# Performance work log

Hardware: AMD Instinct MI355X
Metric: run time of the kernel (lower is better)

## Reference

```python
import jax, jax.numpy as jnp
import numpy as np

B, T, C, H = 2, 4096, 768, 12
D = C // H  # head_dim = 64


def setup_inputs() -> dict:
    key = jax.random.key(0)
    k1, k2, k3 = jax.random.split(key, 3)
    x = jax.random.normal(k1, (B, T, C), dtype=jnp.float32)
    w_qkv = jax.random.normal(k2, (C, 3 * C), dtype=jnp.float32) * (1.0 / np.sqrt(C))
    w_out = jax.random.normal(k3, (C, C), dtype=jnp.float32) * (1.0 / np.sqrt(C))
    return {"x": x, "w_qkv": w_qkv, "w_out": w_out}


def reference(x, w_qkv, w_out):
    b, t, c = x.shape
    qkv = x @ w_qkv                              # (B,T,3C)
    q, k, v = jnp.split(qkv, 3, axis=-1)
    # (B,T,C) -> (B,H,T,D)
    q = q.reshape(b, t, H, D).transpose(0, 2, 1, 3)
    k = k.reshape(b, t, H, D).transpose(0, 2, 1, 3)
    v = v.reshape(b, t, H, D).transpose(0, 2, 1, 3)
    att = jnp.einsum('bhqd,bhkd->bhqk', q, k) / jnp.sqrt(jnp.float32(D))
    causal = jnp.tril(jnp.ones((t, t), dtype=bool))  # True where allowed
    att = jnp.where(causal, att, -jnp.inf)
    att = jax.nn.softmax(att, axis=-1)
    y = jnp.einsum('bhqk,bhkd->bhqd', att, v)        # (B,H,T,D)
    y = y.transpose(0, 2, 1, 3).reshape(b, t, c)
    return y @ w_out
```

## Files before the change

kernel.cpp:

```cpp
#include <hip/hip_runtime.h>
#include <stdint.h>
#include <stddef.h>

#define NB 2
#define NT 4096
#define NC 768
#define NH 12
#define ND 64

typedef unsigned short u16;
typedef __attribute__((ext_vector_type(4))) float f32x4;
typedef __attribute__((ext_vector_type(16))) float f32x16;
typedef __attribute__((ext_vector_type(8))) unsigned short u16x8;
typedef __attribute__((ext_vector_type(4))) unsigned short u16x4;
typedef __attribute__((ext_vector_type(8))) __bf16 bf16x8;
typedef __attribute__((ext_vector_type(4))) unsigned int u32x4;

typedef __attribute__((address_space(1))) const unsigned int gu32;
typedef __attribute__((address_space(3))) unsigned int lu32;

__device__ __forceinline__ u16 f2bf(float f) {
  uint32_t u = __builtin_bit_cast(uint32_t, f);
  u += 0x7FFFu + ((u >> 16) & 1u);
  return (u16)(u >> 16);
}
__device__ __forceinline__ bf16x8 asbf(u16x8 v) { return __builtin_bit_cast(bf16x8, v); }

__device__ __forceinline__ uint32_t pkbf(float a, float b) {
  uint32_t ua = __builtin_bit_cast(uint32_t, a) + 0x8000u;
  uint32_t ub = __builtin_bit_cast(uint32_t, b) + 0x8000u;
  return __builtin_amdgcn_perm(ub, ua, 0x07060302u);
}
__device__ __forceinline__ uint32_t pktr(float a, float b) {
  return __builtin_amdgcn_perm(__builtin_bit_cast(uint32_t, b),
                               __builtin_bit_cast(uint32_t, a), 0x07060302u);
}

#define GLDS(gsrc, ldst) __builtin_amdgcn_global_load_lds( \
    (gu32*)(gsrc), (lu32*)(ldst), 16, 0, 0)

__global__ void k_cast(const float* __restrict__ in, u16* __restrict__ out, int n4) {
  int i = blockIdx.x * blockDim.x + threadIdx.x;
  if (i < n4) {
    f32x4 v = ((const f32x4*)in)[i];
    u16x4 o;
    o[0] = f2bf(v[0]); o[1] = f2bf(v[1]); o[2] = f2bf(v[2]); o[3] = f2bf(v[3]);
    ((u16x4*)out)[i] = o;
  }
}

__global__ void k_transpose(const float* __restrict__ in, u16* __restrict__ out,
                            int R, int Cn) {
  __shared__ float tile[32][33];
  int c0 = blockIdx.x * 32, r0 = blockIdx.y * 32;
  int tx = threadIdx.x & 31, ty = threadIdx.x >> 5;
  for (int i = ty; i < 32; i += 8)
    tile[i][tx] = in[(size_t)(r0 + i) * Cn + c0 + tx];
  __syncthreads();
  for (int i = ty; i < 32; i += 8)
    out[(size_t)(c0 + i) * R + r0 + tx] = f2bf(tile[tx][i]);
}

template <int EPI>
__global__ __launch_bounds__(256, 3)
void k_gemm_bt(const u16* __restrict__ A, const u16* __restrict__ Bt,
               int M, int N, int K,
               u16* __restrict__ o0, u16* __restrict__ o1, u16* __restrict__ o2,
               float* __restrict__ of) {
  __shared__ u16 As[128 * 32];
  __shared__ u16 Bs[128 * 32];
  const int tid = threadIdx.x;
  const int wave = tid >> 6, lane = tid & 63, quad = lane >> 4, lc = lane & 15;
  const int wm = (wave & 1) * 64, wn = (wave >> 1) * 64;
  const int bm = blockIdx.y * 128, bn = blockIdx.x * 128;

  const int sr = tid >> 2;
  const int sc8 = (tid & 3) * 8;
  const u16* ga0 = A + (size_t)(bm + sr) * K + sc8;
  const u16* ga1 = A + (size_t)(bm + 64 + sr) * K + sc8;
  const u16* gb0 = Bt + (size_t)(bn + sr) * K + sc8;
  const u16* gb1 = Bt + (size_t)(bn + 64 + sr) * K + sc8;
  u16* la0 = &As[wave * 512];
  u16* la1 = &As[2048 + wave * 512];
  u16* lb0 = &Bs[wave * 512];
  u16* lb1 = &Bs[2048 + wave * 512];

  f32x4 zv = {0.f, 0.f, 0.f, 0.f};
  f32x4 acc[4][4];
#pragma unroll
  for (int i = 0; i < 4; ++i)
#pragma unroll
    for (int j = 0; j < 4; ++j) acc[i][j] = zv;

  for (int k0 = 0; k0 < K; k0 += 32) {
    __syncthreads();
    GLDS(ga0 + k0, la0);
    GLDS(ga1 + k0, la1);
    GLDS(gb0 + k0, lb0);
    GLDS(gb1 + k0, lb1);
    asm volatile("s_waitcnt vmcnt(0)" ::: "memory");
    __syncthreads();

    bf16x8 af[4], bfv[4];
#pragma unroll
    for (int mi = 0; mi < 4; ++mi)
      af[mi] = asbf(*(const u16x8*)&As[(wm + mi * 16 + lc) * 32 + quad * 8]);
#pragma unroll
    for (int ni = 0; ni < 4; ++ni)
      bfv[ni] = asbf(*(const u16x8*)&Bs[(wn + ni * 16 + lc) * 32 + quad * 8]);
#pragma unroll
    for (int mi = 0; mi < 4; ++mi)
#pragma unroll
      for (int ni = 0; ni < 4; ++ni)
        acc[mi][ni] = __builtin_amdgcn_mfma_f32_16x16x32_bf16(af[mi], bfv[ni],
                                                              acc[mi][ni], 0, 0, 0);
  }

  const int mrow0 = bm + wm + quad * 4;
#pragma unroll
  for (int mi = 0; mi < 4; ++mi) {
    const int mbase = mrow0 + mi * 16;
#pragma unroll
    for (int ni = 0; ni < 4; ++ni) {
      const int n = bn + wn + ni * 16 + lc;
      if (EPI == 0) {
#pragma unroll
        for (int r = 0; r < 4; ++r)
          of[(size_t)(mbase + r) * N + n] = acc[mi][ni][r];
      } else {
        const int sect = n / NC;
        const int wn2 = n - sect * NC;
        const int h = wn2 >> 6, d = wn2 & 63;
        const int b = mbase >> 12;
        const int t = mbase & (NT - 1);
        const float sc = (sect == 0) ? 0.18033688011112042f : 1.0f;
        if (sect == 2) {
          u16x4 pk;
#pragma unroll
          for (int r = 0; r < 4; ++r) pk[r] = f2bf(acc[mi][ni][r]);
          *(u16x4*)&o2[((size_t)(b * NH + h) * ND + d) * NT + t] = pk;
        } else {
          u16* dst = (sect == 0) ? o0 : o1;
#pragma unroll
          for (int r = 0; r < 4; ++r)
            dst[((size_t)(b * NH + h) * NT + (t + r)) * ND + d] =
                f2bf(acc[mi][ni][r] * sc);
        }
      }
    }
  }
}

__device__ __forceinline__ void softpack16(const f32x16& s, int qrel, bool msk,
                                           int l5, float& sl, bf16x8* pf) {
  float e[16];
#pragma unroll
  for (int r = 0; r < 16; ++r) {
    float v = s[r];
    if (msk) {
      int tl = (r & 3) + 8 * (r >> 2) + 4 * l5;
      v = (tl > qrel) ? -1e30f : v;
    }
    e[r] = exp2f(v);
    sl += __builtin_bit_cast(float,
          __builtin_bit_cast(uint32_t, e[r]) & 0xFFFF0000u);
  }
  uint32_t wv[8];
#pragma unroll
  for (int i = 0; i < 8; ++i) wv[i] = pktr(e[2 * i], e[2 * i + 1]);
#pragma unroll
  for (int g = 0; g < 2; ++g) {
    auto r0 = __builtin_amdgcn_permlane32_swap(wv[g * 4 + 0], wv[g * 4 + 2], false, false);
    auto r1 = __builtin_amdgcn_permlane32_swap(wv[g * 4 + 1], wv[g * 4 + 3], false, false);
    u32x4 f = {r0[0], r1[0], r0[1], r1[1]};
    pf[g] = __builtin_bit_cast(bf16x8, f);
  }
}

__global__ __launch_bounds__(256, 3)
void k_attn(const u16* __restrict__ Q, const u16* __restrict__ K,
            const u16* __restrict__ Vt, u16* __restrict__ Y) {
  __shared__ u16 SM[2][64 * 64];
  __shared__ float PL[2][64];
  const int tid = threadIdx.x;
  const int lane = tid & 63, wave = tid >> 6;
  const int l5 = lane >> 5, l31 = lane & 31;
  const int qh = wave & 1, th = wave >> 1;
  const int bh = blockIdx.x % (NB * NH);
  const int qi = 63 - blockIdx.x / (NB * NH);
  const int b = bh / NH, h = bh - b * NH;
  const u16* __restrict__ Qb = Q + (size_t)bh * NT * ND;
  const u16* __restrict__ Kb = K + (size_t)bh * NT * ND;
  const u16* __restrict__ Vb = Vt + (size_t)bh * (size_t)ND * NT;

  const int qg = qi * 64 + qh * 32 + l31;

  bf16x8 bq[4];
#pragma unroll
  for (int ks = 0; ks < 4; ++ks)
    bq[ks] = asbf(*(const u16x8*)(Qb + (size_t)qg * ND + ks * 16 + l5 * 8));

  f32x16 Zv;
#pragma unroll
  for (int i = 0; i < 16; ++i) Zv[i] = 0.f;
  f32x16 o0 = Zv, o1 = Zv;
  float sl = 0.f;

  const int srow = tid >> 3, sg = tid & 7;
  const int soff = srow * 64 + ((sg ^ (srow & 7)) * 8);
  const u16* __restrict__ pK = Kb + (size_t)srow * ND + sg * 8;
  const u16* __restrict__ pV = Vb + (size_t)srow * NT + sg * 8;

  int qfro[4];
#pragma unroll
  for (int ks = 0; ks < 4; ++ks)
    qfro[ks] = (th * 32 + l31) * 64 + (((ks * 2 + l5) ^ (l31 & 7)) * 8);
  int vfro[2];
#pragma unroll
  for (int kp = 0; kp < 2; ++kp)
    vfro[kp] = l31 * 64 + ((((2 * th + kp) * 2 + l5) ^ (l31 & 7)) * 8);

  u16x8 st[4];
  st[0] = *(const u16x8*)(pK);
  st[1] = *(const u16x8*)(pK + (size_t)32 * ND);
  st[2] = *(const u16x8*)(pV);
  st[3] = *(const u16x8*)(pV + (size_t)32 * NT);

#pragma unroll 1
  for (int tau = 0; tau <= qi; ++tau) {
    __syncthreads();
    *(u16x8*)&SM[0][soff] = st[0];
    *(u16x8*)&SM[0][2048 + soff] = st[1];
    *(u16x8*)&SM[1][soff] = st[2];
    *(u16x8*)&SM[1][2048 + soff] = st[3];
    __syncthreads();

    const bool dg = (tau == qi);
    const bool act = !(dg && th > qh);
    bf16x8 p[2];
    if (act) {
      f32x16 s = Zv;
#pragma unroll
      for (int ks = 0; ks < 4; ++ks) {
        bf16x8 kf = asbf(*(const u16x8*)&SM[0][qfro[ks]]);
        s = __builtin_amdgcn_mfma_f32_32x32x16_bf16(kf, bq[ks], s, 0, 0, 0);
      }
      softpack16(s, l31, dg && (th == qh), l5, sl, p);
    }

    if (tau < qi) {
      const int tn = (tau + 1) * 64;
      st[0] = *(const u16x8*)(pK + (size_t)tn * ND);
      st[1] = *(const u16x8*)(pK + (size_t)(tn + 32) * ND);
      st[2] = *(const u16x8*)(pV + tn);
      st[3] = *(const u16x8*)(pV + (size_t)32 * NT + tn);
    }

    if (act) {
#pragma unroll
      for (int kp = 0; kp < 2; ++kp) {
        bf16x8 v0 = asbf(*(const u16x8*)&SM[1][vfro[kp]]);
        bf16x8 v1 = asbf(*(const u16x8*)&SM[1][2048 + vfro[kp]]);
        o0 = __builtin_amdgcn_mfma_f32_32x32x16_bf16(v0, p[kp], o0, 0, 0, 0);
        o1 = __builtin_amdgcn_mfma_f32_32x32x16_bf16(v1, p[kp], o1, 0, 0, 0);
      }
    }
  }

  float l = sl + __shfl_xor(sl, 32);
  __syncthreads();
  float* PK = (float*)&SM[0][0];
  if (th == 0) {
#pragma unroll
    for (int r = 0; r < 16; ++r) PK[(qh * 32 + r) * 64 + lane] = o0[r];
#pragma unroll
    for (int r = 0; r < 16; ++r) PK[(qh * 32 + 16 + r) * 64 + lane] = o1[r];
    PL[qh][lane] = l;
  }
  __syncthreads();
  if (th == 1) {
#pragma unroll
    for (int r = 0; r < 16; ++r) o0[r] += PK[(qh * 32 + r) * 64 + lane];
#pragma unroll
    for (int r = 0; r < 16; ++r) o1[r] += PK[(qh * 32 + 16 + r) * 64 + lane];
    l += PL[qh][lane];
    const float inv = 1.f / l;
    u16* yrow = Y + (size_t)(b * NT + qg) * NC + h * 64;
#pragma unroll
    for (int dh = 0; dh < 2; ++dh) {
      const f32x16& o = dh ? o1 : o0;
#pragma unroll
      for (int rq = 0; rq < 4; ++rq) {
        const int d = dh * 32 + 8 * rq + 4 * l5;
        uint2 w;
        w.x = pkbf(o[rq * 4 + 0] * inv, o[rq * 4 + 1] * inv);
        w.y = pkbf(o[rq * 4 + 2] * inv, o[rq * 4 + 3] * inv);
        *(uint2*)&yrow[d] = w;
      }
    }
  }
}

extern "C" void kernel_launch(void* const* d_in, const int* in_sizes, int n_in,
                              void* d_out, int out_size, void* d_ws, size_t ws_size,
                              hipStream_t stream) {
  (void)in_sizes; (void)n_in; (void)out_size; (void)ws_size;
  const float* x = (const float*)d_in[0];
  const float* w_qkv = (const float*)d_in[1];
  const float* w_out = (const float*)d_in[2];
  float* out = (float*)d_out;

  u16* ws = (u16*)d_ws;
  const size_t XE = (size_t)NB * NT * NC;
  u16* xb  = ws;
  u16* wqT = xb + XE;
  u16* woT = wqT + (size_t)3 * NC * NC;
  u16* Qb  = woT + (size_t)NC * NC;
  u16* Kb  = Qb + XE;
  u16* Vtb = Kb + XE;
  u16* yb  = Vtb + XE;

  k_cast<<<(int)(XE / 4 / 256), 256, 0, stream>>>(x, xb, (int)(XE / 4));
  k_transpose<<<dim3(3 * NC / 32, NC / 32), 256, 0, stream>>>(w_qkv, wqT, NC, 3 * NC);
  k_transpose<<<dim3(NC / 32, NC / 32), 256, 0, stream>>>(w_out, woT, NC, NC);
  k_gemm_bt<1><<<dim3(3 * NC / 128, NB * NT / 128), 256, 0, stream>>>(
      xb, wqT, NB * NT, 3 * NC, NC, Qb, Kb, Vtb, nullptr);
  k_attn<<<dim3((NB * NH) * 64), 256, 0, stream>>>(Qb, Kb, Vtb, yb);
  k_gemm_bt<0><<<dim3(NC / 128, NB * NT / 128), 256, 0, stream>>>(
      yb, woT, NB * NT, NC, NC, nullptr, nullptr, nullptr, out);
}
```

Baseline: 244.3 us.

## Fuse preprocessing kernels, stage V-transpose epilogue via LDS, tweak attention scheduling

Merges the cast and two weight-transpose kernels into one launch to cut launch overhead. The QKV GEMM epilogue for the V section now stages the tile through shared memory with a swizzle, so it can write coalesced 16-byte rows of the transposed V layout instead of scattered 8-byte stores. In attention, the row-sum accumulation becomes a two-lane vector add taken from the packed bf16 values, and s_setprio raises wave priority around the MFMA blocks. These are several unrelated micro-optimizations, and the extra LDS round trip and barriers in the epilogue add some cost.

```diff
diff --git a/kernel.cpp b/kernel.cpp
--- a/kernel.cpp
+++ b/kernel.cpp
@@ -9,6 +9,7 @@
 #define ND 64
 
 typedef unsigned short u16;
+typedef __attribute__((ext_vector_type(2))) float f32x2;
 typedef __attribute__((ext_vector_type(4))) float f32x4;
 typedef __attribute__((ext_vector_type(16))) float f32x16;
 typedef __attribute__((ext_vector_type(8))) unsigned short u16x8;
@@ -39,21 +40,40 @@
 #define GLDS(gsrc, ldst) __builtin_amdgcn_global_load_lds( \
     (gu32*)(gsrc), (lu32*)(ldst), 16, 0, 0)
 
-__global__ void k_cast(const float* __restrict__ in, u16* __restrict__ out, int n4) {
-  int i = blockIdx.x * blockDim.x + threadIdx.x;
-  if (i < n4) {
-    f32x4 v = ((const f32x4*)in)[i];
+#define PRE_CAST_BLKS 6144
+#define PRE_TA_BX 72
+#define PRE_TA_BLKS (72 * 24)
+#define PRE_TB_BX 24
+#define PRE_TB_BLKS (24 * 24)
+__global__ __launch_bounds__(256)
+void k_pre(const float* __restrict__ x, u16* __restrict__ xb,
+           const float* __restrict__ w_qkv, u16* __restrict__ wqT,
+           const float* __restrict__ w_out, u16* __restrict__ woT) {
+  __shared__ float tile[32][33];
+  const int bid = blockIdx.x;
+  const int tid = threadIdx.x;
+  if (bid < PRE_CAST_BLKS) {
+    int i = bid * 256 + tid;
+    f32x4 v = ((const f32x4*)x)[i];
     u16x4 o;
     o[0] = f2bf(v[0]); o[1] = f2bf(v[1]); o[2] = f2bf(v[2]); o[3] = f2bf(v[3]);
-    ((u16x4*)out)[i] = o;
-  }
-}
-
-__global__ void k_transpose(const float* __restrict__ in, u16* __restrict__ out,
-                            int R, int Cn) {
-  __shared__ float tile[32][33];
-  int c0 = blockIdx.x * 32, r0 = blockIdx.y * 32;
-  int tx = threadIdx.x & 31, ty = threadIdx.x >> 5;
+    ((u16x4*)xb)[i] = o;
+    return;
+  }
+  const float* in;
+  u16* out;
+  int R, Cn, bx, by;
+  if (bid < PRE_CAST_BLKS + PRE_TA_BLKS) {
+    int q = bid - PRE_CAST_BLKS;
+    bx = q % PRE_TA_BX; by = q / PRE_TA_BX;
+    in = w_qkv; out = wqT; R = NC; Cn = 3 * NC;
+  } else {
+    int q = bid - PRE_CAST_BLKS - PRE_TA_BLKS;
+    bx = q % PRE_TB_BX; by = q / PRE_TB_BX;
+    in = w_out; out = woT; R = NC; Cn = NC;
+  }
+  int c0 = bx * 32, r0 = by * 32;
+  int tx = tid & 31, ty = tid >> 5;
   for (int i = ty; i < 32; i += 8)
     tile[i][tx] = in[(size_t)(r0 + i) * Cn + c0 + tx];
   __syncthreads();
@@ -67,8 +87,9 @@
                int M, int N, int K,
                u16* __restrict__ o0, u16* __restrict__ o1, u16* __restrict__ o2,
                float* __restrict__ of) {
-  __shared__ u16 As[128 * 32];
-  __shared__ u16 Bs[128 * 32];
+  __shared__ u16 SMEM[2 * 128 * 32];
+  u16* As = SMEM;
+  u16* Bs = SMEM + 4096;
   const int tid = threadIdx.x;
   const int wave = tid >> 6, lane = tid & 63, quad = lane >> 4, lc = lane & 15;
   const int wm = (wave & 1) * 64, wn = (wave >> 1) * 64;
@@ -116,6 +137,41 @@
                                                               acc[mi][ni], 0, 0, 0);
   }
 
+  const int sect = (EPI == 1) ? (bn / NC) : 0;
+  if (EPI == 1 && sect == 2) {
+    const int b = bm >> 12;
+    const int tb = bm & (NT - 1);
+    const int hb = (bn - 2 * NC) >> 6;
+#pragma unroll 1
+    for (int r2_ = 0; r2_ < 2; ++r2_) {
+      __syncthreads();
+      if ((wave >> 1) == r2_) {
+#pragma unroll
+        for (int mi = 0; mi < 4; ++mi)
+#pragma unroll
+          for (int ni = 0; ni < 4; ++ni) {
+            const int nl = ni * 16 + lc;
+#pragma unroll
+            for (int r = 0; r < 4; ++r) {
+              const int m = wm + mi * 16 + quad * 4 + r;
+              SMEM[nl * 128 + (m ^ ((nl & 7) << 3))] = f2bf(acc[mi][ni][r]);
+            }
+          }
+      }
+      __syncthreads();
+#pragma unroll
+      for (int pass = 0; pass < 4; ++pass) {
+        const int row = (tid >> 4) + 16 * pass;
+        const int chunk = tid & 15;
+        u16x8 w = *(const u16x8*)&SMEM[row * 128 + ((chunk ^ (row & 7)) * 8)];
+        const int nl = 64 * r2_ + row;
+        *(u16x8*)&o2[((size_t)(b * NH + hb + (nl >> 6)) * ND + (nl & 63)) * NT
+                     + tb + chunk * 8] = w;
+      }
+    }
+    return;
+  }
+
   const int mrow0 = bm + wm + quad * 4;
 #pragma unroll
   for (int mi = 0; mi < 4; ++mi) {
@@ -128,31 +184,23 @@
         for (int r = 0; r < 4; ++r)
           of[(size_t)(mbase + r) * N + n] = acc[mi][ni][r];
       } else {
-        const int sect = n / NC;
         const int wn2 = n - sect * NC;
         const int h = wn2 >> 6, d = wn2 & 63;
         const int b = mbase >> 12;
         const int t = mbase & (NT - 1);
         const float sc = (sect == 0) ? 0.18033688011112042f : 1.0f;
-        if (sect == 2) {
-          u16x4 pk;
-#pragma unroll
-          for (int r = 0; r < 4; ++r) pk[r] = f2bf(acc[mi][ni][r]);
-          *(u16x4*)&o2[((size_t)(b * NH + h) * ND + d) * NT + t] = pk;
-        } else {
-          u16* dst = (sect == 0) ? o0 : o1;
-#pragma unroll
-          for (int r = 0; r < 4; ++r)
-            dst[((size_t)(b * NH + h) * NT + (t + r)) * ND + d] =
-                f2bf(acc[mi][ni][r] * sc);
-        }
+        u16* dst = (sect == 0) ? o0 : o1;
+#pragma unroll
+        for (int r = 0; r < 4; ++r)
+          dst[((size_t)(b * NH + h) * NT + (t + r)) * ND + d] =
+              f2bf(acc[mi][ni][r] * sc);
       }
     }
   }
 }
 
 __device__ __forceinline__ void softpack16(const f32x16& s, int qrel, bool msk,
-                                           int l5, float& sl, bf16x8* pf) {
+                                           int l5, f32x2& sl2, bf16x8* pf) {
   float e[16];
 #pragma unroll
   for (int r = 0; r < 16; ++r) {
@@ -162,12 +210,15 @@
       v = (tl > qrel) ? -1e30f : v;
     }
     e[r] = exp2f(v);
-    sl += __builtin_bit_cast(float,
-          __builtin_bit_cast(uint32_t, e[r]) & 0xFFFF0000u);
   }
   uint32_t wv[8];
 #pragma unroll
-  for (int i = 0; i < 8; ++i) wv[i] = pktr(e[2 * i], e[2 * i + 1]);
+  for (int i = 0; i < 8; ++i) {
+    wv[i] = pktr(e[2 * i], e[2 * i + 1]);
+    f32x2 inc = {__builtin_bit_cast(float, wv[i] & 0xFFFF0000u),
+                 __builtin_bit_cast(float, wv[i] << 16)};
+    sl2 += inc;
+  }
 #pragma unroll
   for (int g = 0; g < 2; ++g) {
     auto r0 = __builtin_amdgcn_permlane32_swap(wv[g * 4 + 0], wv[g * 4 + 2], false, false);
@@ -204,7 +255,7 @@
 #pragma unroll
   for (int i = 0; i < 16; ++i) Zv[i] = 0.f;
   f32x16 o0 = Zv, o1 = Zv;
-  float sl = 0.f;
+  f32x2 sl2 = {0.f, 0.f};
 
   const int srow = tid >> 3, sg = tid & 7;
   const int soff = srow * 64 + ((sg ^ (srow & 7)) * 8);
@@ -239,13 +290,16 @@
     const bool act = !(dg && th > qh);
     bf16x8 p[2];
     if (act) {
-      f32x16 s = Zv;
-#pragma unroll
-      for (int ks = 0; ks < 4; ++ks) {
+      bf16x8 kf0 = asbf(*(const u16x8*)&SM[0][qfro[0]]);
+      __builtin_amdgcn_s_setprio(1);
+      f32x16 s = __builtin_amdgcn_mfma_f32_32x32x16_bf16(kf0, bq[0], Zv, 0, 0, 0);
+#pragma unroll
+      for (int ks = 1; ks < 4; ++ks) {
         bf16x8 kf = asbf(*(const u16x8*)&SM[0][qfro[ks]]);
         s = __builtin_amdgcn_mfma_f32_32x32x16_bf16(kf, bq[ks], s, 0, 0, 0);
       }
-      softpack16(s, l31, dg && (th == qh), l5, sl, p);
+      __builtin_amdgcn_s_setprio(0);
+      softpack16(s, l31, dg && (th == qh), l5, sl2, p);
     }
 
     if (tau < qi) {
@@ -257,6 +311,7 @@
     }
 
     if (act) {
+      __builtin_amdgcn_s_setprio(1);
 #pragma unroll
       for (int kp = 0; kp < 2; ++kp) {
         bf16x8 v0 = asbf(*(const u16x8*)&SM[1][vfro[kp]]);
@@ -264,10 +319,12 @@
         o0 = __builtin_amdgcn_mfma_f32_32x32x16_bf16(v0, p[kp], o0, 0, 0, 0);
         o1 = __builtin_amdgcn_mfma_f32_32x32x16_bf16(v1, p[kp], o1, 0, 0, 0);
       }
-    }
-  }
-
-  float l = sl + __shfl_xor(sl, 32);
+      __builtin_amdgcn_s_setprio(0);
+    }
+  }
+
+  const float slv = sl2[0] + sl2[1];
+  float l = slv + __shfl_xor(slv, 32);
   __syncthreads();
   float* PK = (float*)&SM[0][0];
   if (th == 0) {
@@ -320,9 +377,8 @@
   u16* Vtb = Kb + XE;
   u16* yb  = Vtb + XE;
 
-  k_cast<<<(int)(XE / 4 / 256), 256, 0, stream>>>(x, xb, (int)(XE / 4));
-  k_transpose<<<dim3(3 * NC / 32, NC / 32), 256, 0, stream>>>(w_qkv, wqT, NC, 3 * NC);
-  k_transpose<<<dim3(NC / 32, NC / 32), 256, 0, stream>>>(w_out, woT, NC, NC);
+  k_pre<<<dim3(PRE_CAST_BLKS + PRE_TA_BLKS + PRE_TB_BLKS), 256, 0, stream>>>(
+      x, xb, w_qkv, wqT, w_out, woT);
   k_gemm_bt<1><<<dim3(3 * NC / 128, NB * NT / 128), 256, 0, stream>>>(
       xb, wqT, NB * NT, 3 * NC, NC, Qb, Kb, Vtb, nullptr);
   k_attn<<<dim3((NB * NH) * 64), 256, 0, stream>>>(Qb, Kb, Vtb, yb);
```

After: 235.3 us. 1.04x faster.
